# Optimization experiments

Measured on AMD Instinct MI355X. Metric: run time of the kernel, lower is better.

The kernel has to match this reference:

```python
import jax, jax.numpy as jnp
import numpy as np

ENCODER_DIM, DECODER_DIM, ATTN_DIM = 2048, 512, 512
B, P = 128, 196  # batch, num_pixels (14x14)


def setup_inputs() -> dict:
    key = jax.random.key(0)
    ks = jax.random.split(key, 8)
    s_e = 1.0 / np.sqrt(ENCODER_DIM)
    s_d = 1.0 / np.sqrt(DECODER_DIM)
    s_a = 1.0 / np.sqrt(ATTN_DIM)
    return {
        "encoder_out": jax.random.normal(ks[0], (B, P, ENCODER_DIM), jnp.float32),
        "decoder_hidden": jax.random.normal(ks[1], (B, DECODER_DIM), jnp.float32),
        "W_enc": jax.random.uniform(ks[2], (ENCODER_DIM, ATTN_DIM), jnp.float32, -s_e, s_e),
        "b_enc": jax.random.uniform(ks[3], (ATTN_DIM,), jnp.float32, -s_e, s_e),
        "W_dec": jax.random.uniform(ks[4], (DECODER_DIM, ATTN_DIM), jnp.float32, -s_d, s_d),
        "b_dec": jax.random.uniform(ks[5], (ATTN_DIM,), jnp.float32, -s_d, s_d),
        "W_full": jax.random.uniform(ks[6], (ATTN_DIM,), jnp.float32, -s_a, s_a),
        "b_full": jax.random.uniform(ks[7], (), jnp.float32, -s_a, s_a),
    }


def reference(encoder_out, decoder_hidden, W_enc, b_enc, W_dec, b_dec, W_full, b_full):
    # att1: [B, P, A]; att2: [B, A]
    att1 = jnp.einsum("bpe,ea->bpa", encoder_out, W_enc) + b_enc
    att2 = decoder_hidden @ W_dec + b_dec
    # broadcast add + relu + score projection -> [B, P]
    att = jax.nn.relu(att1 + att2[:, None, :]) @ W_full + b_full
    alpha = jax.nn.softmax(att, axis=1)  # over pixels
    # weighted sum over pixels -> [B, E]
    attention_weighted_encoding = jnp.einsum("bpe,bp->be", encoder_out, alpha)
    return (attention_weighted_encoding, alpha)
```

## Files before the change

kernel.cpp:

```cpp
#include <hip/hip_runtime.h>
#include <hip/hip_bf16.h>

#define ENC_DIM 2048
#define DEC_DIM 512
#define ATT_DIM 512
#define BATCH   128
#define NPIX    196
#define NROWS   (BATCH * NPIX)

typedef short bf16x8 __attribute__((ext_vector_type(8)));
typedef float f32x4  __attribute__((ext_vector_type(4)));
typedef unsigned short u16x8 __attribute__((ext_vector_type(8)));

__device__ __forceinline__ unsigned short f2bf(float f) {
    union { float f; unsigned u; } v; v.f = f;
    unsigned r = v.u + 0x7fffu + ((v.u >> 16) & 1u);
    return (unsigned short)(r >> 16);
}

__device__ __forceinline__ short bfc(float f) {
    union { __hip_bfloat16 h; short s; } v;
    v.h = __float2bfloat16(f);
    return v.s;
}

__device__ __forceinline__ void gload16(const void* g, void* l) {
    __builtin_amdgcn_global_load_lds(
        (const __attribute__((address_space(1))) unsigned int*)g,
        (__attribute__((address_space(3))) unsigned int*)l, 16, 0, 0);
}

__global__ void prep(const float* __restrict__ W_enc, const float* __restrict__ dh,
                     const float* __restrict__ W_dec, const float* __restrict__ b_dec,
                     const float* __restrict__ b_enc, const float* __restrict__ b_full,
                     unsigned short* __restrict__ Wt, float* __restrict__ att2,
                     float* __restrict__ score) {
    __shared__ float ts[64][65];
    const int bid = blockIdx.x, t = threadIdx.x;

    if (bid < 98) score[bid * 256 + t] = b_full[0];

    if (bid < 256) {
        const int a0 = (bid & 7) * 64;
        const int e0 = (bid >> 3) * 64;
        const int tx = t & 15;
        const int ty = t >> 4;
        #pragma unroll
        for (int p = 0; p < 4; ++p) {
            const int e = ty + p * 16;
            const float4 v = *(const float4*)&W_enc[(size_t)(e0 + e) * ATT_DIM + a0 + tx * 4];
            ts[e][tx * 4 + 0] = v.x; ts[e][tx * 4 + 1] = v.y;
            ts[e][tx * 4 + 2] = v.z; ts[e][tx * 4 + 3] = v.w;
        }
        __syncthreads();
        #pragma unroll
        for (int p = 0; p < 4; ++p) {
            const int a = ty + p * 16;
            ushort4 u;
            u.x = f2bf(ts[tx * 4 + 0][a]);
            u.y = f2bf(ts[tx * 4 + 1][a]);
            u.z = f2bf(ts[tx * 4 + 2][a]);
            u.w = f2bf(ts[tx * 4 + 3][a]);
            *(ushort4*)&Wt[(size_t)(a0 + a) * ENC_DIM + e0 + tx * 4] = u;
        }
    } else {
        float* dhs = &ts[0][0];
        const int kb = bid - 256;
        const int b  = kb >> 1;
        const int c  = (kb & 1) * 256 + t;
        dhs[t]       = dh[b * DEC_DIM + t];
        dhs[t + 256] = dh[b * DEC_DIM + t + 256];
        __syncthreads();
        float acc0 = 0.f, acc1 = 0.f;
        #pragma unroll 8
        for (int d = 0; d < 256; ++d) {
            acc0 += dhs[d]       * W_dec[d * ATT_DIM + c];
            acc1 += dhs[d + 256] * W_dec[(d + 256) * ATT_DIM + c];
        }
        att2[b * ATT_DIM + c] = acc0 + acc1 + b_dec[c] + b_enc[c];
    }
}

__launch_bounds__(256, 3)
__global__ void k2_gemm(const float* __restrict__ enc, const unsigned short* __restrict__ Wt,
                        const float* __restrict__ att2, const float* __restrict__ W_full,
                        float* __restrict__ score) {
    __shared__ __align__(16) float          Asf[128 * 64];
    __shared__ __align__(16) unsigned short Bs [128 * 64];
    __shared__ float att2s[2][128];
    __shared__ float wfs[128];

    const int t = threadIdx.x;
    const int tile = (blockIdx.x & 7) * 98 + (blockIdx.x >> 3);
    const int n0   = (tile & 3) * 128;
    const int row0 = (tile >> 2) * 128;
    const int b0   = row0 / NPIX;
    const int rows_left = (b0 + 1) * NPIX - row0;

    if (t < 128) {
        att2s[0][t] = att2[b0 * ATT_DIM + n0 + t];
        att2s[1][t] = (b0 + 1 < BATCH) ? att2[(b0 + 1) * ATT_DIM + n0 + t] : 0.f;
        wfs[t]      = W_full[n0 + t];
    }

    const int w    = t >> 6;
    const int lane = t & 63;
    const int q    = lane >> 4;
    const int cl   = lane & 15;
    const int wm   = (w >> 1) * 64;
    const int wn   = (w & 1) * 64;

    f32x4 acc[4][4] = {};

    const int r4 = lane >> 4;
    const int sl = lane & 15;
    const float* aS0 = enc + (size_t)(row0 + w * 32 + r4)     * ENC_DIM + ((sl ^ r4)       << 2);
    const float* aS1 = enc + (size_t)(row0 + w * 32 + 4 + r4) * ENC_DIM + ((sl ^ (4 + r4)) << 2);

    const int br = lane >> 3;
    const int bc = ((lane & 7) ^ br) * 8;
    const unsigned short* WtB = Wt + (size_t)(n0 + w * 32 + br) * ENC_DIM + bc;

    unsigned ab[4], ab2[4];
    #pragma unroll
    for (int mi = 0; mi < 4; ++mi) {
        unsigned base = ((unsigned)(wm + mi * 16 + cl) << 8) + ((unsigned)(cl & 7) << 4);
        base ^= (unsigned)(q << 5);
        ab[mi]  = base;
        ab2[mi] = base ^ 16u;
    }
    const char* Ab = (const char*)Asf;

    for (int kk = 0; kk < ENC_DIM; kk += 64) {
        __syncthreads();
        #pragma unroll
        for (int i = 0; i < 4; ++i)
            gload16(WtB + (size_t)i * 8 * ENC_DIM + kk, &Bs[(w * 32 + i * 8) * 64]);
        #pragma unroll
        for (int i = 0; i < 4; ++i) {
            gload16(aS0 + (size_t)i * 8 * ENC_DIM + kk, &Asf[(w * 32 + i * 8)     * 64]);
            gload16(aS1 + (size_t)i * 8 * ENC_DIM + kk, &Asf[(w * 32 + i * 8 + 4) * 64]);
        }
        __syncthreads();

        #pragma unroll
        for (int h = 0; h < 2; ++h) {
            bf16x8 af[4], bfr[4];
            #pragma unroll
            for (int mi = 0; mi < 4; ++mi) {
                const f32x4 fa = *(const f32x4*)(Ab + ab[mi]  + h * 128);
                const f32x4 fb = *(const f32x4*)(Ab + ab2[mi] + h * 128);
                bf16x8 u;
                u[0] = bfc(fa[0]); u[1] = bfc(fa[1]); u[2] = bfc(fa[2]); u[3] = bfc(fa[3]);
                u[4] = bfc(fb[0]); u[5] = bfc(fb[1]); u[6] = bfc(fb[2]); u[7] = bfc(fb[3]);
                af[mi] = u;
            }
            #pragma unroll
            for (int i = 0; i < 4; ++i)
                bfr[i] = *(const bf16x8*)&Bs[(wn + i * 16 + cl) * 64
                                             + (((h * 4 + q) ^ (cl & 7)) * 8)];
            #pragma unroll
            for (int mi = 0; mi < 4; ++mi)
                #pragma unroll
                for (int ni = 0; ni < 4; ++ni)
                    acc[mi][ni] = __builtin_amdgcn_mfma_f32_16x16x32_bf16(
                        af[mi], bfr[ni], acc[mi][ni], 0, 0, 0);
        }
    }

    #pragma unroll
    for (int mi = 0; mi < 4; ++mi) {
        float rs[4];
        #pragma unroll
        for (int i = 0; i < 4; ++i) {
            const int lr  = wm + mi * 16 + q * 4 + i;
            const int sel = (lr >= rows_left) ? 1 : 0;
            float sum = 0.f;
            #pragma unroll
            for (int ni = 0; ni < 4; ++ni) {
                const int j = wn + ni * 16 + cl;
                float v = acc[mi][ni][i] + att2s[sel][j];
                v = fmaxf(v, 0.f);
                sum += v * wfs[j];
            }
            rs[i] = sum;
        }
        #pragma unroll
        for (int o = 1; o < 16; o <<= 1) {
            #pragma unroll
            for (int i = 0; i < 4; ++i) rs[i] += __shfl_xor(rs[i], o);
        }
        if (cl == 0) {
            #pragma unroll
            for (int i = 0; i < 4; ++i) {
                const int r = row0 + wm + mi * 16 + q * 4 + i;
                atomicAdd(&score[r], rs[i]);
            }
        }
    }
}

__global__ void k4_awe(const float* __restrict__ enc, const float* __restrict__ score,
                       float* __restrict__ alpha, float* __restrict__ awe) {
    __shared__ float as[NPIX];
    __shared__ float red[4];
    __shared__ f32x4 redv[4][64];
    const int b  = blockIdx.y;
    const int t  = threadIdx.x;
    const int wv = t >> 6, lane = t & 63;
    const float x = (t < NPIX) ? score[b * NPIX + t] : -INFINITY;
    float m = x;
    #pragma unroll
    for (int o = 32; o >= 1; o >>= 1) m = fmaxf(m, __shfl_xor(m, o));
    if (lane == 0) red[wv] = m;
    __syncthreads();
    m = fmaxf(fmaxf(red[0], red[1]), fmaxf(red[2], red[3]));
    const float e = (t < NPIX) ? __expf(x - m) : 0.f;
    float s = e;
    #pragma unroll
    for (int o = 32; o >= 1; o >>= 1) s += __shfl_xor(s, o);
    __syncthreads();
    if (lane == 0) red[wv] = s;
    __syncthreads();
    s = red[0] + red[1] + red[2] + red[3];
    const float a = e / s;
    if (t < NPIX) {
        as[t] = a;
        if (blockIdx.x == 0) alpha[b * NPIX + t] = a;
    }
    __syncthreads();
    const int e0 = blockIdx.x * 256 + lane * 4;
    const float* base = enc + (size_t)b * NPIX * ENC_DIM + e0;
    f32x4 a0 = {}, a1 = {}, a2 = {}, a3 = {};
    int p = wv;
    #pragma unroll 4
    for (int it = 0; it < 12; ++it, p += 16) {
        a0 += as[p]      * *(const f32x4*)(base + (size_t)(p)      * ENC_DIM);
        a1 += as[p + 4]  * *(const f32x4*)(base + (size_t)(p + 4)  * ENC_DIM);
        a2 += as[p + 8]  * *(const f32x4*)(base + (size_t)(p + 8)  * ENC_DIM);
        a3 += as[p + 12] * *(const f32x4*)(base + (size_t)(p + 12) * ENC_DIM);
    }
    a0 += as[p] * *(const f32x4*)(base + (size_t)p * ENC_DIM);
    redv[wv][lane] = (a0 + a1) + (a2 + a3);
    __syncthreads();
    if (wv == 0) {
        const f32x4 r = (redv[0][lane] + redv[1][lane]) + (redv[2][lane] + redv[3][lane]);
        *(f32x4*)&awe[(size_t)b * ENC_DIM + e0] = r;
    }
}

extern "C" void kernel_launch(void* const* d_in, const int* in_sizes, int n_in,
                              void* d_out, int out_size, void* d_ws, size_t ws_size,
                              hipStream_t stream) {
    const float* enc    = (const float*)d_in[0];
    const float* dh     = (const float*)d_in[1];
    const float* W_enc  = (const float*)d_in[2];
    const float* b_enc  = (const float*)d_in[3];
    const float* W_dec  = (const float*)d_in[4];
    const float* b_dec  = (const float*)d_in[5];
    const float* W_full = (const float*)d_in[6];
    const float* b_full = (const float*)d_in[7];

    float* awe   = (float*)d_out;
    float* alpha = awe + BATCH * ENC_DIM;

    unsigned short* Wt    = (unsigned short*)d_ws;
    float*          att2  = (float*)((char*)d_ws + (size_t)ATT_DIM * ENC_DIM * 2);
    float*          score = att2 + (size_t)BATCH * ATT_DIM;

    prep   <<<512,          256, 0, stream>>>(W_enc, dh, W_dec, b_dec, b_enc, b_full,
                                              Wt, att2, score);
    k2_gemm<<<784,          256, 0, stream>>>(enc, Wt, att2, W_full, score);
    k4_awe <<<dim3(8, 128), 256, 0, stream>>>(enc, score, alpha, awe);
}
```

Baseline: 391.2 us.

## Prefetch next K tile into registers and double-buffer B in shared memory

Measured after the change: 427.0 us. 9.2% more time.

```diff
diff --git a/kernel.cpp b/kernel.cpp
--- a/kernel.cpp
+++ b/kernel.cpp
@@ -18,10 +18,10 @@
     return (unsigned short)(r >> 16);
 }
 
-__device__ __forceinline__ short bfc(float f) {
-    union { __hip_bfloat16 h; short s; } v;
+__device__ __forceinline__ unsigned short bfc(float f) {
+    union { __hip_bfloat16 h; unsigned short u; } v;
     v.h = __float2bfloat16(f);
-    return v.s;
+    return v.u;
 }
 
 __device__ __forceinline__ void gload16(const void* g, void* l) {
@@ -85,8 +85,8 @@
 __global__ void k2_gemm(const float* __restrict__ enc, const unsigned short* __restrict__ Wt,
                         const float* __restrict__ att2, const float* __restrict__ W_full,
                         float* __restrict__ score) {
-    __shared__ __align__(16) float          Asf[128 * 64];
-    __shared__ __align__(16) unsigned short Bs [128 * 64];
+    __shared__ __align__(16) unsigned short As[128 * 72];
+    __shared__ __align__(16) unsigned short Bs[2][128 * 64];
     __shared__ float att2s[2][128];
     __shared__ float wfs[128];
 
@@ -112,59 +112,86 @@
 
     f32x4 acc[4][4] = {};
 
-    const int r4 = lane >> 4;
-    const int sl = lane & 15;
-    const float* aS0 = enc + (size_t)(row0 + w * 32 + r4)     * ENC_DIM + ((sl ^ r4)       << 2);
-    const float* aS1 = enc + (size_t)(row0 + w * 32 + 4 + r4) * ENC_DIM + ((sl ^ (4 + r4)) << 2);
+    const int ar = t >> 3;
+    const int ak = (t & 7) * 8;
+    const float* encA = enc + (size_t)(row0 + ar) * ENC_DIM + ak;
 
     const int br = lane >> 3;
     const int bc = ((lane & 7) ^ br) * 8;
     const unsigned short* WtB = Wt + (size_t)(n0 + w * 32 + br) * ENC_DIM + bc;
 
-    unsigned ab[4], ab2[4];
-    #pragma unroll
-    for (int mi = 0; mi < 4; ++mi) {
-        unsigned base = ((unsigned)(wm + mi * 16 + cl) << 8) + ((unsigned)(cl & 7) << 4);
-        base ^= (unsigned)(q << 5);
-        ab[mi]  = base;
-        ab2[mi] = base ^ 16u;
-    }
-    const char* Ab = (const char*)Asf;
-
-    for (int kk = 0; kk < ENC_DIM; kk += 64) {
-        __syncthreads();
+    {
         #pragma unroll
         for (int i = 0; i < 4; ++i)
-            gload16(WtB + (size_t)i * 8 * ENC_DIM + kk, &Bs[(w * 32 + i * 8) * 64]);
-        #pragma unroll
-        for (int i = 0; i < 4; ++i) {
-            gload16(aS0 + (size_t)i * 8 * ENC_DIM + kk, &Asf[(w * 32 + i * 8)     * 64]);
-            gload16(aS1 + (size_t)i * 8 * ENC_DIM + kk, &Asf[(w * 32 + i * 8 + 4) * 64]);
-        }
-        __syncthreads();
+            gload16(WtB + (size_t)i * 8 * ENC_DIM, &Bs[0][(w * 32 + i * 8) * 64]);
+        #pragma unroll
+        for (int p = 0; p < 4; ++p) {
+            const float4 v0 = *(const float4*)(encA + (size_t)p * 32 * ENC_DIM);
+            const float4 v1 = *(const float4*)(encA + (size_t)p * 32 * ENC_DIM + 4);
+            u16x8 u;
+            u[0] = bfc(v0.x); u[1] = bfc(v0.y); u[2] = bfc(v0.z); u[3] = bfc(v0.w);
+            u[4] = bfc(v1.x); u[5] = bfc(v1.y); u[6] = bfc(v1.z); u[7] = bfc(v1.w);
+            *(u16x8*)&As[(ar + p * 32) * 72 + ak] = u;
+        }
+    }
+    __syncthreads();
+
+    int cur = 0;
+    for (int kk = 0; kk < ENC_DIM; kk += 64, cur ^= 1) {
+        const int  nxt = cur ^ 1;
+        const bool pf  = (kk + 64 < ENC_DIM);
+        float4 aL0, aL1, aL2, aL3, aL4, aL5, aL6, aL7;
+
+        if (pf) {
+            #pragma unroll
+            for (int i = 0; i < 4; ++i)
+                gload16(WtB + (size_t)i * 8 * ENC_DIM + kk + 64,
+                        &Bs[nxt][(w * 32 + i * 8) * 64]);
+            aL0 = *(const float4*)(encA + (size_t)0 * 32 * ENC_DIM + kk + 64);
+            aL1 = *(const float4*)(encA + (size_t)0 * 32 * ENC_DIM + kk + 68);
+            aL2 = *(const float4*)(encA + (size_t)1 * 32 * ENC_DIM + kk + 64);
+            aL3 = *(const float4*)(encA + (size_t)1 * 32 * ENC_DIM + kk + 68);
+            aL4 = *(const float4*)(encA + (size_t)2 * 32 * ENC_DIM + kk + 64);
+            aL5 = *(const float4*)(encA + (size_t)2 * 32 * ENC_DIM + kk + 68);
+            aL6 = *(const float4*)(encA + (size_t)3 * 32 * ENC_DIM + kk + 64);
+            aL7 = *(const float4*)(encA + (size_t)3 * 32 * ENC_DIM + kk + 68);
+        }
 
         #pragma unroll
         for (int h = 0; h < 2; ++h) {
             bf16x8 af[4], bfr[4];
             #pragma unroll
-            for (int mi = 0; mi < 4; ++mi) {
-                const f32x4 fa = *(const f32x4*)(Ab + ab[mi]  + h * 128);
-                const f32x4 fb = *(const f32x4*)(Ab + ab2[mi] + h * 128);
-                bf16x8 u;
-                u[0] = bfc(fa[0]); u[1] = bfc(fa[1]); u[2] = bfc(fa[2]); u[3] = bfc(fa[3]);
-                u[4] = bfc(fb[0]); u[5] = bfc(fb[1]); u[6] = bfc(fb[2]); u[7] = bfc(fb[3]);
-                af[mi] = u;
-            }
-            #pragma unroll
             for (int i = 0; i < 4; ++i)
-                bfr[i] = *(const bf16x8*)&Bs[(wn + i * 16 + cl) * 64
-                                             + (((h * 4 + q) ^ (cl & 7)) * 8)];
+                af[i]  = *(const bf16x8*)&As[(wm + i * 16 + cl) * 72 + h * 32 + q * 8];
+            #pragma unroll
+            for (int i = 0; i < 4; ++i)
+                bfr[i] = *(const bf16x8*)&Bs[cur][(wn + i * 16 + cl) * 64
+                                                  + (((h * 4 + q) ^ (cl & 7)) * 8)];
             #pragma unroll
             for (int mi = 0; mi < 4; ++mi)
                 #pragma unroll
                 for (int ni = 0; ni < 4; ++ni)
                     acc[mi][ni] = __builtin_amdgcn_mfma_f32_16x16x32_bf16(
                         af[mi], bfr[ni], acc[mi][ni], 0, 0, 0);
+        }
+
+        __syncthreads();
+
+        if (pf) {
+            u16x8 u0, u1, u2, u3;
+            u0[0]=bfc(aL0.x); u0[1]=bfc(aL0.y); u0[2]=bfc(aL0.z); u0[3]=bfc(aL0.w);
+            u0[4]=bfc(aL1.x); u0[5]=bfc(aL1.y); u0[6]=bfc(aL1.z); u0[7]=bfc(aL1.w);
+            u1[0]=bfc(aL2.x); u1[1]=bfc(aL2.y); u1[2]=bfc(aL2.z); u1[3]=bfc(aL2.w);
+            u1[4]=bfc(aL3.x); u1[5]=bfc(aL3.y); u1[6]=bfc(aL3.z); u1[7]=bfc(aL3.w);
+            u2[0]=bfc(aL4.x); u2[1]=bfc(aL4.y); u2[2]=bfc(aL4.z); u2[3]=bfc(aL4.w);
+            u2[4]=bfc(aL5.x); u2[5]=bfc(aL5.y); u2[6]=bfc(aL5.z); u2[7]=bfc(aL5.w);
+            u3[0]=bfc(aL6.x); u3[1]=bfc(aL6.y); u3[2]=bfc(aL6.z); u3[3]=bfc(aL6.w);
+            u3[4]=bfc(aL7.x); u3[5]=bfc(aL7.y); u3[6]=bfc(aL7.z); u3[7]=bfc(aL7.w);
+            *(u16x8*)&As[(ar +  0) * 72 + ak] = u0;
+            *(u16x8*)&As[(ar + 32) * 72 + ak] = u1;
+            *(u16x8*)&As[(ar + 64) * 72 + ak] = u2;
+            *(u16x8*)&As[(ar + 96) * 72 + ak] = u3;
+            __syncthreads();
         }
     }
 
```

## Load GEMM operands directly from global memory instead of staging in LDS

Applied to the files above, without the earlier changes.

New measurement: 619.5 us. 58.4% more time.

```diff
diff --git a/kernel.cpp b/kernel.cpp
--- a/kernel.cpp
+++ b/kernel.cpp
@@ -18,16 +18,10 @@
     return (unsigned short)(r >> 16);
 }
 
-__device__ __forceinline__ short bfc(float f) {
-    union { __hip_bfloat16 h; short s; } v;
+__device__ __forceinline__ unsigned short bfc(float f) {
+    union { __hip_bfloat16 h; unsigned short u; } v;
     v.h = __float2bfloat16(f);
-    return v.s;
-}
-
-__device__ __forceinline__ void gload16(const void* g, void* l) {
-    __builtin_amdgcn_global_load_lds(
-        (const __attribute__((address_space(1))) unsigned int*)g,
-        (__attribute__((address_space(3))) unsigned int*)l, 16, 0, 0);
+    return v.u;
 }
 
 __global__ void prep(const float* __restrict__ W_enc, const float* __restrict__ dh,
@@ -85,8 +79,6 @@
 __global__ void k2_gemm(const float* __restrict__ enc, const unsigned short* __restrict__ Wt,
                         const float* __restrict__ att2, const float* __restrict__ W_full,
                         float* __restrict__ score) {
-    __shared__ __align__(16) float          Asf[128 * 64];
-    __shared__ __align__(16) unsigned short Bs [128 * 64];
     __shared__ float att2s[2][128];
     __shared__ float wfs[128];
 
@@ -112,53 +104,30 @@
 
     f32x4 acc[4][4] = {};
 
-    const int r4 = lane >> 4;
-    const int sl = lane & 15;
-    const float* aS0 = enc + (size_t)(row0 + w * 32 + r4)     * ENC_DIM + ((sl ^ r4)       << 2);
-    const float* aS1 = enc + (size_t)(row0 + w * 32 + 4 + r4) * ENC_DIM + ((sl ^ (4 + r4)) << 2);
-
-    const int br = lane >> 3;
-    const int bc = ((lane & 7) ^ br) * 8;
-    const unsigned short* WtB = Wt + (size_t)(n0 + w * 32 + br) * ENC_DIM + bc;
-
-    unsigned ab[4], ab2[4];
-    #pragma unroll
-    for (int mi = 0; mi < 4; ++mi) {
-        unsigned base = ((unsigned)(wm + mi * 16 + cl) << 8) + ((unsigned)(cl & 7) << 4);
-        base ^= (unsigned)(q << 5);
-        ab[mi]  = base;
-        ab2[mi] = base ^ 16u;
-    }
-    const char* Ab = (const char*)Asf;
+    const float* aB[4];
+    const unsigned short* bB[4];
+    #pragma unroll
+    for (int i = 0; i < 4; ++i) {
+        aB[i] = enc + (size_t)(row0 + wm + i * 16 + cl) * ENC_DIM + q * 8;
+        bB[i] = Wt  + (size_t)(n0  + wn + i * 16 + cl) * ENC_DIM + q * 8;
+    }
 
     for (int kk = 0; kk < ENC_DIM; kk += 64) {
-        __syncthreads();
-        #pragma unroll
-        for (int i = 0; i < 4; ++i)
-            gload16(WtB + (size_t)i * 8 * ENC_DIM + kk, &Bs[(w * 32 + i * 8) * 64]);
-        #pragma unroll
-        for (int i = 0; i < 4; ++i) {
-            gload16(aS0 + (size_t)i * 8 * ENC_DIM + kk, &Asf[(w * 32 + i * 8)     * 64]);
-            gload16(aS1 + (size_t)i * 8 * ENC_DIM + kk, &Asf[(w * 32 + i * 8 + 4) * 64]);
-        }
-        __syncthreads();
-
         #pragma unroll
         for (int h = 0; h < 2; ++h) {
             bf16x8 af[4], bfr[4];
             #pragma unroll
             for (int mi = 0; mi < 4; ++mi) {
-                const f32x4 fa = *(const f32x4*)(Ab + ab[mi]  + h * 128);
-                const f32x4 fb = *(const f32x4*)(Ab + ab2[mi] + h * 128);
+                const f32x4 lo = *(const f32x4*)(aB[mi] + kk + h * 32);
+                const f32x4 hi = *(const f32x4*)(aB[mi] + kk + h * 32 + 4);
                 bf16x8 u;
-                u[0] = bfc(fa[0]); u[1] = bfc(fa[1]); u[2] = bfc(fa[2]); u[3] = bfc(fa[3]);
-                u[4] = bfc(fb[0]); u[5] = bfc(fb[1]); u[6] = bfc(fb[2]); u[7] = bfc(fb[3]);
+                u[0] = bfc(lo[0]); u[1] = bfc(lo[1]); u[2] = bfc(lo[2]); u[3] = bfc(lo[3]);
+                u[4] = bfc(hi[0]); u[5] = bfc(hi[1]); u[6] = bfc(hi[2]); u[7] = bfc(hi[3]);
                 af[mi] = u;
             }
             #pragma unroll
-            for (int i = 0; i < 4; ++i)
-                bfr[i] = *(const bf16x8*)&Bs[(wn + i * 16 + cl) * 64
-                                             + (((h * 4 + q) ^ (cl & 7)) * 8)];
+            for (int ni = 0; ni < 4; ++ni)
+                bfr[ni] = *(const bf16x8*)(bB[ni] + kk + h * 32);
             #pragma unroll
             for (int mi = 0; mi < 4; ++mi)
                 #pragma unroll
@@ -167,6 +136,8 @@
                         af[mi], bfr[ni], acc[mi][ni], 0, 0, 0);
         }
     }
+
+    __syncthreads();
 
     #pragma unroll
     for (int mi = 0; mi < 4; ++mi) {
```
